# Kernel optimization log

Hardware: AMD Instinct MI355X
Metric: run time of the kernel (lower is better)

## Reference

```python
import jax, jax.numpy as jnp
import numpy as np

H = 128  # hidden_size hard-coded in AttentionSeqModel


def setup_inputs() -> dict:
    key = jax.random.key(0)
    ks = jax.random.split(key, 20)
    B, L, D, A = 512, 512, 128, 16  # batch, num_light, obs_size, action_size

    def p(k, shape, s=0.05):
        return jax.random.normal(k, shape, dtype=jnp.float32) * s

    return {
        "obs": jax.random.normal(ks[0], (B, L, D), dtype=jnp.float32),
        # encoder params
        "enc_emb_W": p(ks[1], (H, D)), "enc_emb_b": p(ks[2], (H,)),
        "enc_Wih": p(ks[3], (3 * H, H)), "enc_Whh": p(ks[4], (3 * H, H)),
        "enc_bih": p(ks[5], (3 * H,)), "enc_bhh": p(ks[6], (3 * H,)),
        # decoder params
        "dec_emb_W": p(ks[7], (H, A)), "dec_emb_b": p(ks[8], (H,)),
        "attn_W": p(ks[9], (L, 2 * H)), "attn_b": p(ks[10], (L,)),
        "comb_W": p(ks[11], (H, 2 * H)), "comb_b": p(ks[12], (H,)),
        "dec_Wih": p(ks[13], (3 * H, H)), "dec_Whh": p(ks[14], (3 * H, H)),
        "dec_bih": p(ks[15], (3 * H,)), "dec_bhh": p(ks[16], (3 * H,)),
        "out_W": p(ks[17], (A, H)), "out_b": p(ks[18], (A,)),
    }


def _gru_cell(x, h, Wih, Whh, bih, bhh):
    # torch.nn.GRU single-step semantics
    gi = x @ Wih.T + bih          # (B, 3H)
    gh = h @ Whh.T + bhh          # (B, 3H)
    ir, iz, inn = jnp.split(gi, 3, axis=-1)
    hr, hz, hn = jnp.split(gh, 3, axis=-1)
    r = jax.nn.sigmoid(ir + hr)
    z = jax.nn.sigmoid(iz + hz)
    n = jnp.tanh(inn + r * hn)
    return (1.0 - z) * n + z * h


def reference(obs, enc_emb_W, enc_emb_b, enc_Wih, enc_Whh, enc_bih, enc_bhh,
              dec_emb_W, dec_emb_b, attn_W, attn_b, comb_W, comb_b,
              dec_Wih, dec_Whh, dec_bih, dec_bhh, out_W, out_b):
    B, L, _ = obs.shape
    A = out_b.shape[0]

    # ---- encoder loop over num_light timesteps ----
    def enc_step(h, x_t):
        emb = x_t @ enc_emb_W.T + enc_emb_b           # (B, H)
        h2 = _gru_cell(emb, h, enc_Wih, enc_Whh, enc_bih, enc_bhh)
        # original stores encoder_output[0, 0]: only batch element 0
        return h2, h2[0]

    h0 = jnp.zeros((B, H), obs.dtype)
    hN, enc_outs = jax.lax.scan(enc_step, h0, jnp.swapaxes(obs, 0, 1))
    # enc_outs: (L, H)

    # ---- decoder loop, feeding log-softmax logits back as input ----
    def dec_step(carry, _):
        inp, h = carry
        emb = inp @ dec_emb_W.T + dec_emb_b           # (B, H); dropout = identity (eval)
        aw = jax.nn.softmax(jnp.concatenate([emb, h], axis=1) @ attn_W.T + attn_b, axis=1)  # (B, L)
        applied = aw @ enc_outs                        # (B, H)
        o = jax.nn.relu(jnp.concatenate([emb, applied], axis=1) @ comb_W.T + comb_b)
        h2 = _gru_cell(o, h, dec_Wih, dec_Whh, dec_bih, dec_bhh)
        logits = jax.nn.log_softmax(h2 @ out_W.T + out_b, axis=1)  # (B, A)
        return (logits, h2), None

    init = (jnp.zeros((B, A), obs.dtype), hN)
    (logits, _), _ = jax.lax.scan(dec_step, init, None, length=L)
    return logits
```

## Files before the change

kernel.cpp:

```cpp
#include <hip/hip_runtime.h>
#include <stdint.h>

#define H_  128
#define L_  512
#define B_  512
#define A_  16
#define G3_ 384

#define OFF_M1    0
#define OFF_WHHE  98304
#define OFF_WB    196608
#define OFF_WIH   327680
#define OFF_WHH   425984
#define OFF_WC2   524288
#define OFF_PA    557056
#define OFF_PC    573440
#define OFF_OUTW  577536
#define OFF_BGI   581632
#define OFF_ZB    583168
#define OFF_OB    585216
#define OFF_ENC   585728
#define OFF_HN    716800

typedef _Float16 f16_t;
typedef __attribute__((ext_vector_type(2))) _Float16 f16x2_t;

__device__ __forceinline__ float dot2f(uint32_t w, uint32_t a, float acc) {
#if __has_builtin(__builtin_amdgcn_fdot2)
  return __builtin_amdgcn_fdot2(__builtin_bit_cast(f16x2_t, w),
                                __builtin_bit_cast(f16x2_t, a), acc, false);
#else
  f16x2_t x = __builtin_bit_cast(f16x2_t, w);
  f16x2_t y = __builtin_bit_cast(f16x2_t, a);
  return acc + (float)x.x * (float)y.x + (float)x.y * (float)y.y;
#endif
}

__device__ __forceinline__ uint32_t pk2(float lo, float hi) {
#if __has_builtin(__builtin_amdgcn_cvt_pkrtz)
  return __builtin_bit_cast(uint32_t, __builtin_amdgcn_cvt_pkrtz(lo, hi));
#else
  f16x2_t v; v.x = (_Float16)lo; v.y = (_Float16)hi;
  return __builtin_bit_cast(uint32_t, v);
#endif
}

__device__ __forceinline__ float sigm(float x) { return 1.f / (1.f + __expf(-x)); }
__device__ __forceinline__ float tanh_s(float t) { float ex = __expf(2.f * t); return 1.f - 2.f / (ex + 1.f); }

#define LDS4(arr, idx) (*(const uint4*)&(arr)[(idx)])

__global__ void prep_kernel(const float* __restrict__ enc_emb_W, const float* __restrict__ enc_emb_b,
                            const float* __restrict__ enc_Wih, const float* __restrict__ enc_bih,
                            const float* __restrict__ dec_emb_W, const float* __restrict__ dec_emb_b,
                            const float* __restrict__ attn_W, const float* __restrict__ attn_b,
                            const float* __restrict__ comb_W, const float* __restrict__ comb_b,
                            const float* __restrict__ dec_Wih, const float* __restrict__ dec_Whh,
                            const float* __restrict__ enc_Whh, const float* __restrict__ out_W,
                            char* __restrict__ ws) {
  int t = blockIdx.x * 256 + threadIdx.x;
  if (t < 49152) {
    int n = t >> 7, d = t & 127; float acc = 0.f;
    for (int h = 0; h < 128; ++h) acc += enc_Wih[n*128+h] * enc_emb_W[h*128+d];
    ((f16_t*)(ws+OFF_M1))[t] = (f16_t)acc; return;
  } t -= 49152;
  if (t < 384) {
    float acc = enc_bih[t];
    for (int h = 0; h < 128; ++h) acc += enc_Wih[t*128+h] * enc_emb_b[h];
    ((float*)(ws+OFF_BGI))[t] = acc; return;
  } t -= 384;
  if (t < 8192) {
    int l = t >> 4, a = t & 15; float acc = 0.f;
    for (int k = 0; k < 128; ++k) acc += attn_W[l*256+k] * dec_emb_W[k*16+a];
    ((f16_t*)(ws+OFF_PA))[t] = (f16_t)acc; return;
  } t -= 8192;
  if (t < 512) {
    float acc = attn_b[t];
    for (int k = 0; k < 128; ++k) acc += attn_W[t*256+k] * dec_emb_b[k];
    ((float*)(ws+OFF_ZB))[t] = acc; return;
  } t -= 512;
  if (t < 2048) {
    int j = t >> 4, a = t & 15; float acc = 0.f;
    for (int k = 0; k < 128; ++k) acc += comb_W[j*256+k] * dec_emb_W[k*16+a];
    ((f16_t*)(ws+OFF_PC))[t] = (f16_t)acc; return;
  } t -= 2048;
  if (t < 128) {
    float acc = comb_b[t];
    for (int k = 0; k < 128; ++k) acc += comb_W[t*256+k] * dec_emb_b[k];
    ((float*)(ws+OFF_OB))[t] = acc; return;
  } t -= 128;
  if (t < 65536) {
    int l = t >> 7, k = t & 127;
    ((f16_t*)(ws+OFF_WB))[t] = (f16_t)attn_W[l*256+128+k]; return;
  } t -= 65536;
  if (t < 49152) { ((f16_t*)(ws+OFF_WHHE))[t] = (f16_t)enc_Whh[t]; return; } t -= 49152;
  if (t < 49152) { ((f16_t*)(ws+OFF_WIH))[t]  = (f16_t)dec_Wih[t]; return; } t -= 49152;
  if (t < 49152) { ((f16_t*)(ws+OFF_WHH))[t]  = (f16_t)dec_Whh[t]; return; } t -= 49152;
  if (t < 16384) {
    int j = t >> 7, k = t & 127;
    ((f16_t*)(ws+OFF_WC2))[t] = (f16_t)comb_W[j*256+128+k]; return;
  } t -= 16384;
  if (t < 2048) { ((f16_t*)(ws+OFF_OUTW))[t] = (f16_t)out_W[t]; return; }
}

__global__ __launch_bounds__(512, 1) void enc_kernel(const float* __restrict__ obs,
                                                     const float* __restrict__ enc_bhh,
                                                     char* __restrict__ ws) {
  __shared__ __align__(16) uint32_t obspk[2][64];
  __shared__ __align__(16) uint32_t hpk[2][64];
  __shared__ __align__(16) float    gi_s[2][G3_];
  __shared__ __align__(16) float    gh_s[2][G3_];
  __shared__ float bgi_s[G3_], bhh_s[G3_];

  const int tid = threadIdx.x, bid = blockIdx.x;
  const uint32_t* M1u  = (const uint32_t*)(ws + OFF_M1);
  const uint32_t* WHu  = (const uint32_t*)(ws + OFF_WHHE);
  const float*    bgi  = (const float*)(ws + OFF_BGI);
  f16_t* encw = (f16_t*)(ws + OFF_ENC);
  float* hN   = (float*)(ws + OFF_HN);

  uint32_t m1r[64], whr[64];
  if (tid < G3_) {
    const uint4* p1 = (const uint4*)(M1u + tid*64);
    const uint4* p2 = (const uint4*)(WHu + tid*64);
#pragma unroll
    for (int q = 0; q < 16; ++q) {
      uint4 v = p1[q]; m1r[q*4]=v.x; m1r[q*4+1]=v.y; m1r[q*4+2]=v.z; m1r[q*4+3]=v.w;
      uint4 w = p2[q]; whr[q*4]=w.x; whr[q*4+1]=w.y; whr[q*4+2]=w.z; whr[q*4+3]=w.w;
    }
    bgi_s[tid] = bgi[tid]; bhh_s[tid] = enc_bhh[tid];
  }

  const int r = tid >> 7, jj = tid & 127;
  const size_t rowbase = (size_t)(2*bid + r) * L_ * H_ + jj;
  float hreg = 0.f;
  float oA = 0.f;
  if (tid < 256) {
    float o0 = obs[rowbase + 0*H_];
    float op = __shfl_xor(o0, 1);
    if (!(jj & 1)) obspk[r][jj >> 1] = pk2(o0, op);
    oA = obs[rowbase + 1*H_];
  }
  if (tid < 128) hpk[tid>>6][tid&63] = 0u;
  __syncthreads();

#pragma unroll 1
  for (int t = 0; t < L_; ++t) {
    float oB = 0.f;
    if (tid < 256) {
      int tn = (t+2 < L_) ? t+2 : L_-1;
      oB = obs[rowbase + (size_t)tn*H_];
    }
    if (tid < G3_) {
      float g0 = bgi_s[tid], g1 = g0, ga = 0.f, gb = 0.f;
      float e0 = bhh_s[tid], e1 = e0, ea = 0.f, eb = 0.f;
#pragma unroll
      for (int c = 0; c < 16; ++c) {
        uint4 o0 = LDS4(obspk[0], c*4); uint4 o1 = LDS4(obspk[1], c*4);
        uint4 h0 = LDS4(hpk[0],  c*4);  uint4 h1 = LDS4(hpk[1],  c*4);
        g0 = dot2f(m1r[c*4+0], o0.x, g0); g0 = dot2f(m1r[c*4+1], o0.y, g0);
        ga = dot2f(m1r[c*4+2], o0.z, ga); ga = dot2f(m1r[c*4+3], o0.w, ga);
        g1 = dot2f(m1r[c*4+0], o1.x, g1); g1 = dot2f(m1r[c*4+1], o1.y, g1);
        gb = dot2f(m1r[c*4+2], o1.z, gb); gb = dot2f(m1r[c*4+3], o1.w, gb);
        e0 = dot2f(whr[c*4+0], h0.x, e0); e0 = dot2f(whr[c*4+1], h0.y, e0);
        ea = dot2f(whr[c*4+2], h0.z, ea); ea = dot2f(whr[c*4+3], h0.w, ea);
        e1 = dot2f(whr[c*4+0], h1.x, e1); e1 = dot2f(whr[c*4+1], h1.y, e1);
        eb = dot2f(whr[c*4+2], h1.z, eb); eb = dot2f(whr[c*4+3], h1.w, eb);
      }
      gi_s[0][tid] = g0+ga; gi_s[1][tid] = g1+gb;
      gh_s[0][tid] = e0+ea; gh_s[1][tid] = e1+eb;
    }
    __syncthreads();
    if (tid < 256) {
      float ir = gi_s[r][jj], iz = gi_s[r][jj+128], in_ = gi_s[r][jj+256];
      float hr = gh_s[r][jj], hz = gh_s[r][jj+128], hn = gh_s[r][jj+256];
      float rg = sigm(ir + hr);
      float zg = sigm(iz + hz);
      float nn = tanh_s(in_ + rg * hn);
      float h2 = (1.f - zg) * nn + zg * hreg;
      hreg = h2;
      float hp = __shfl_xor(h2, 1);
      float op = __shfl_xor(oA, 1);
      if (!(jj & 1)) {
        hpk[r][jj >> 1] = pk2(h2, hp);
        obspk[r][jj >> 1] = pk2(oA, op);
      }
      if (bid == 0 && r == 0) encw[t*H_ + jj] = (f16_t)h2;
      oA = oB;
    }
    __syncthreads();
  }
  if (tid < 256) hN[(2*bid + r)*H_ + jj] = hreg;
}

__global__ __launch_bounds__(512, 1) void dec_kernel(const float* __restrict__ dec_bih,
                                                     const float* __restrict__ dec_bhh,
                                                     const float* __restrict__ out_b,
                                                     char* __restrict__ ws,
                                                     float* __restrict__ dout) {
  __shared__ __align__(16) uint32_t encI[32768];
  __shared__ __align__(16) uint32_t paL[4096];
  __shared__ __align__(16) uint32_t pcL[1024];
  __shared__ __align__(16) uint32_t owL[1024];
  __shared__ __align__(16) uint32_t awpk[2][272];
  __shared__ __align__(16) uint32_t aplpk[2][64];
  __shared__ __align__(16) uint32_t gip[G3_];
  __shared__ __align__(16) uint32_t ghp[G3_];
  __shared__ __align__(16) uint32_t opk[2][64];
  __shared__ __align__(16) uint32_t hpk[2][64];
  __shared__ __align__(16) uint32_t inppk[2][8];
  __shared__ float redm[2][8], reds[2][8];

  const int tid = threadIdx.x, bid = blockIdx.x;
  const uint32_t* WBu  = (const uint32_t*)(ws + OFF_WB);
  const uint32_t* WIu  = (const uint32_t*)(ws + OFF_WIH);
  const uint32_t* WHu  = (const uint32_t*)(ws + OFF_WHH);
  const uint32_t* WCu  = (const uint32_t*)(ws + OFF_WC2);
  const uint32_t* PAu  = (const uint32_t*)(ws + OFF_PA);
  const uint32_t* PCu  = (const uint32_t*)(ws + OFF_PC);
  const uint32_t* OWu  = (const uint32_t*)(ws + OFF_OUTW);
  const float*    zb   = (const float*)(ws + OFF_ZB);
  const float*    obg  = (const float*)(ws + OFF_OB);
  const float*    hN   = (const float*)(ws + OFF_HN);

  uint32_t wb[64], wA[64], wB[64];
  {
    const uint4* p = (const uint4*)(WBu + tid*64);
#pragma unroll
    for (int q = 0; q < 16; ++q) { uint4 v = p[q]; wb[q*4]=v.x; wb[q*4+1]=v.y; wb[q*4+2]=v.z; wb[q*4+3]=v.w; }
  }
  if (tid < G3_) {
    const uint4* p = (const uint4*)(WIu + tid*64);
    const uint4* p2 = (const uint4*)(WHu + tid*64);
#pragma unroll
    for (int q = 0; q < 16; ++q) {
      uint4 v = p[q];  wA[q*4]=v.x; wA[q*4+1]=v.y; wA[q*4+2]=v.z; wA[q*4+3]=v.w;
      uint4 w = p2[q]; wB[q*4]=w.x; wB[q*4+1]=w.y; wB[q*4+2]=w.z; wB[q*4+3]=w.w;
    }
  } else {
    const uint4* p = (const uint4*)(WCu + (tid-384)*64);
#pragma unroll
    for (int q = 0; q < 16; ++q) {
      uint4 v = p[q]; wA[q*4]=v.x; wA[q*4+1]=v.y; wA[q*4+2]=v.z; wA[q*4+3]=v.w;
    }
  }

  {
    int k = tid & 127, ls = tid >> 7;
    const uint16_t* eg = (const uint16_t*)(ws + OFF_ENC);
    uint16_t* ei = (uint16_t*)encI;
    for (int cc = 0; cc < 16; ++cc) {
      int c = ls*16 + cc;
#pragma unroll
      for (int p = 0; p < 8; ++p) ei[(c*128 + k)*8 + p] = eg[(c*8 + p)*128 + k];
    }
  }
  for (int idx = tid; idx < 4096; idx += 512) {
    int q = idx >> 9, l = idx & 511;
    paL[idx] = PAu[l*8 + q];
  }
  for (int idx = tid; idx < 1024; idx += 512) {
    int q = idx >> 7, j = idx & 127;
    pcL[idx] = PCu[j*8 + q];
    int qq = idx & 3, rest = idx >> 2, a = rest & 15, c = rest >> 4;
    owL[(c*16 + a)*4 + qq] = OWu[a*64 + c*4 + qq];
  }
  const float bih_reg  = (tid < G3_) ? dec_bih[tid] : 0.f;
  const float bhh_reg  = (tid < G3_) ? dec_bhh[tid] : 0.f;
  const float ob_reg   = (tid >= G3_) ? obg[tid - G3_] : 0.f;
  const float outb_reg = (tid < 32) ? out_b[tid & 15] : 0.f;
  if (tid < 16) inppk[tid>>3][tid&7] = 0u;

  const int r6 = tid >> 7, j6 = tid & 127;
  float hreg = 0.f;
  if (tid < 256) {
    hreg = hN[(2*bid + r6)*H_ + j6];
    float hp = __shfl_xor(hreg, 1);
    if (!(j6 & 1)) hpk[r6][j6 >> 1] = pk2(hreg, hp);
  }
  const float zbias = zb[tid];
  __syncthreads();

#pragma unroll 1
  for (int t = 0; t < L_; ++t) {
    {
      uint32_t paq[8];
#pragma unroll
      for (int q = 0; q < 8; ++q) paq[q] = paL[q*512 + tid];
      uint4 i0 = LDS4(inppk[0], 0), i0b = LDS4(inppk[0], 4);
      uint4 i1 = LDS4(inppk[1], 0), i1b = LDS4(inppk[1], 4);
      float a0 = dot2f(paq[0], i0.x, zbias); a0 = dot2f(paq[1], i0.y, a0);
      a0 = dot2f(paq[2], i0.z, a0);          a0 = dot2f(paq[3], i0.w, a0);
      float b0 = dot2f(paq[4], i0b.x, 0.f);  b0 = dot2f(paq[5], i0b.y, b0);
      b0 = dot2f(paq[6], i0b.z, b0);         b0 = dot2f(paq[7], i0b.w, b0);
      float a1 = dot2f(paq[0], i1.x, zbias); a1 = dot2f(paq[1], i1.y, a1);
      a1 = dot2f(paq[2], i1.z, a1);          a1 = dot2f(paq[3], i1.w, a1);
      float b1 = dot2f(paq[4], i1b.x, 0.f);  b1 = dot2f(paq[5], i1b.y, b1);
      b1 = dot2f(paq[6], i1b.z, b1);         b1 = dot2f(paq[7], i1b.w, b1);
#pragma unroll
      for (int c = 0; c < 16; ++c) {
        uint4 h0 = LDS4(hpk[0], c*4); uint4 h1 = LDS4(hpk[1], c*4);
        a0 = dot2f(wb[c*4+0], h0.x, a0); a0 = dot2f(wb[c*4+1], h0.y, a0);
        b0 = dot2f(wb[c*4+2], h0.z, b0); b0 = dot2f(wb[c*4+3], h0.w, b0);
        a1 = dot2f(wb[c*4+0], h1.x, a1); a1 = dot2f(wb[c*4+1], h1.y, a1);
        b1 = dot2f(wb[c*4+2], h1.z, b1); b1 = dot2f(wb[c*4+3], h1.w, b1);
      }
      float z0 = a0 + b0, z1 = a1 + b1;
      float m0 = z0, m1 = z1;
#pragma unroll
      for (int off = 32; off; off >>= 1) {
        m0 = fmaxf(m0, __shfl_xor(m0, off));
        m1 = fmaxf(m1, __shfl_xor(m1, off));
      }
      float e0 = __expf(z0 - m0), e1 = __expf(z1 - m1);
      float s0 = e0, s1 = e1;
#pragma unroll
      for (int off = 32; off; off >>= 1) { s0 += __shfl_xor(s0, off); s1 += __shfl_xor(s1, off); }
      int wv = tid >> 6;
      if ((tid & 63) == 0) { redm[0][wv] = m0; redm[1][wv] = m1; reds[0][wv] = s0; reds[1][wv] = s1; }
      float ep0 = __shfl_xor(e0, 1), ep1 = __shfl_xor(e1, 1);
      int awi = (tid >> 1) + ((tid >> 7) << 2);
      if (!(tid & 1)) { awpk[0][awi] = pk2(e0, ep0); awpk[1][awi] = pk2(e1, ep1); }
    }
    __syncthreads();
    {
      int lane = tid & 63, wv3 = tid >> 6;
      int k = wv3*16 + (lane & 15), chunk = lane >> 4;
      float M0 = redm[0][0], M1 = redm[1][0];
#pragma unroll
      for (int i = 1; i < 8; ++i) { M0 = fmaxf(M0, redm[0][i]); M1 = fmaxf(M1, redm[1][i]); }
      float S0 = 0.f, S1 = 0.f;
#pragma unroll
      for (int i = 0; i < 8; ++i) {
        S0 += reds[0][i] * __expf(redm[0][i] - M0);
        S1 += reds[1][i] * __expf(redm[1][i] - M1);
      }
      float is0 = 1.f / S0, is1 = 1.f / S1;
      int cb = chunk*2;
      float sc00 = __expf(redm[0][cb]   - M0) * is0;
      float sc01 = __expf(redm[0][cb+1] - M0) * is0;
      float sc10 = __expf(redm[1][cb]   - M1) * is1;
      float sc11 = __expf(redm[1][cb+1] - M1) * is1;
      int eb0 = chunk*8192 + k*4;
      int awb = chunk*68;
      float a00=0.f, a01=0.f, a10=0.f, a11=0.f;
#pragma unroll
      for (int cc = 0; cc < 8; ++cc) {
        uint4 ev = *(const uint4*)&encI[eb0 + cc*512];
        uint4 w0 = *(const uint4*)&awpk[0][awb + cc*4];
        uint4 wq = *(const uint4*)&awpk[1][awb + cc*4];
        a00 = dot2f(ev.x, w0.x, a00); a00 = dot2f(ev.y, w0.y, a00);
        a00 = dot2f(ev.z, w0.z, a00); a00 = dot2f(ev.w, w0.w, a00);
        a10 = dot2f(ev.x, wq.x, a10); a10 = dot2f(ev.y, wq.y, a10);
        a10 = dot2f(ev.z, wq.z, a10); a10 = dot2f(ev.w, wq.w, a10);
      }
#pragma unroll
      for (int cc = 8; cc < 16; ++cc) {
        uint4 ev = *(const uint4*)&encI[eb0 + cc*512];
        uint4 w0 = *(const uint4*)&awpk[0][awb + cc*4];
        uint4 wq = *(const uint4*)&awpk[1][awb + cc*4];
        a01 = dot2f(ev.x, w0.x, a01); a01 = dot2f(ev.y, w0.y, a01);
        a01 = dot2f(ev.z, w0.z, a01); a01 = dot2f(ev.w, w0.w, a01);
        a11 = dot2f(ev.x, wq.x, a11); a11 = dot2f(ev.y, wq.y, a11);
        a11 = dot2f(ev.z, wq.z, a11); a11 = dot2f(ev.w, wq.w, a11);
      }
      float v0 = a00*sc00 + a01*sc01;
      float v1 = a10*sc10 + a11*sc11;
      v0 += __shfl_xor(v0, 16); v0 += __shfl_xor(v0, 32);
      v1 += __shfl_xor(v1, 16); v1 += __shfl_xor(v1, 32);
      float v0p = __shfl_xor(v0, 1), v1p = __shfl_xor(v1, 1);
      if (!(lane & 49)) {
        int kk = k >> 1;
        aplpk[0][kk] = pk2(v0, v0p); aplpk[1][kk] = pk2(v1, v1p);
      }
    }
    __syncthreads();
    if (tid >= G3_) {
      int jj = tid - G3_;
      uint32_t pcq[8];
#pragma unroll
      for (int q = 0; q < 8; ++q) pcq[q] = pcL[q*128 + jj];
      uint4 i0 = LDS4(inppk[0], 0), i0b = LDS4(inppk[0], 4);
      uint4 i1 = LDS4(inppk[1], 0), i1b = LDS4(inppk[1], 4);
      float o0 = dot2f(pcq[0], i0.x, ob_reg); o0 = dot2f(pcq[1], i0.y, o0);
      o0 = dot2f(pcq[2], i0.z, o0);           o0 = dot2f(pcq[3], i0.w, o0);
      float oa = dot2f(pcq[4], i0b.x, 0.f);   oa = dot2f(pcq[5], i0b.y, oa);
      oa = dot2f(pcq[6], i0b.z, oa);          oa = dot2f(pcq[7], i0b.w, oa);
      float o1 = dot2f(pcq[0], i1.x, ob_reg); o1 = dot2f(pcq[1], i1.y, o1);
      o1 = dot2f(pcq[2], i1.z, o1);           o1 = dot2f(pcq[3], i1.w, o1);
      float obb = dot2f(pcq[4], i1b.x, 0.f);  obb = dot2f(pcq[5], i1b.y, obb);
      obb = dot2f(pcq[6], i1b.z, obb);        obb = dot2f(pcq[7], i1b.w, obb);
#pragma unroll
      for (int c = 0; c < 16; ++c) {
        uint4 p0 = LDS4(aplpk[0], c*4); uint4 p1 = LDS4(aplpk[1], c*4);
        o0 = dot2f(wA[c*4+0], p0.x, o0); o0 = dot2f(wA[c*4+1], p0.y, o0);
        oa = dot2f(wA[c*4+2], p0.z, oa); oa = dot2f(wA[c*4+3], p0.w, oa);
        o1 = dot2f(wA[c*4+0], p1.x, o1); o1 = dot2f(wA[c*4+1], p1.y, o1);
        obb = dot2f(wA[c*4+2], p1.z, obb); obb = dot2f(wA[c*4+3], p1.w, obb);
      }
      o0 = fmaxf(o0 + oa, 0.f); o1 = fmaxf(o1 + obb, 0.f);
      float px0 = __shfl_xor(o0, 1), px1 = __shfl_xor(o1, 1);
      if (!(jj & 1)) { opk[0][jj>>1] = pk2(o0, px0); opk[1][jj>>1] = pk2(o1, px1); }
    } else {
      float e0g = bhh_reg, e1g = e0g, ea = 0.f, eb = 0.f;
#pragma unroll
      for (int c = 0; c < 16; ++c) {
        uint4 h0 = LDS4(hpk[0], c*4); uint4 h1 = LDS4(hpk[1], c*4);
        e0g = dot2f(wB[c*4+0], h0.x, e0g); e0g = dot2f(wB[c*4+1], h0.y, e0g);
        ea  = dot2f(wB[c*4+2], h0.z, ea);  ea  = dot2f(wB[c*4+3], h0.w, ea);
        e1g = dot2f(wB[c*4+0], h1.x, e1g); e1g = dot2f(wB[c*4+1], h1.y, e1g);
        eb  = dot2f(wB[c*4+2], h1.z, eb);  eb  = dot2f(wB[c*4+3], h1.w, eb);
      }
      ghp[tid] = pk2(e0g + ea, e1g + eb);
    }
    __syncthreads();
    if (tid < G3_) {
      float g0 = bih_reg, g1 = g0, ga = 0.f, gb = 0.f;
#pragma unroll
      for (int c = 0; c < 16; ++c) {
        uint4 o0 = LDS4(opk[0], c*4); uint4 o1 = LDS4(opk[1], c*4);
        g0 = dot2f(wA[c*4+0], o0.x, g0); g0 = dot2f(wA[c*4+1], o0.y, g0);
        ga = dot2f(wA[c*4+2], o0.z, ga); ga = dot2f(wA[c*4+3], o0.w, ga);
        g1 = dot2f(wA[c*4+0], o1.x, g1); g1 = dot2f(wA[c*4+1], o1.y, g1);
        gb = dot2f(wA[c*4+2], o1.z, gb); gb = dot2f(wA[c*4+3], o1.w, gb);
      }
      gip[tid] = pk2(g0 + ga, g1 + gb);
    }
    __syncthreads();
    if (tid < 256) {
#define UNPK_(u) (r6 ? (float)(__builtin_bit_cast(f16x2_t,(u)).y) : (float)(__builtin_bit_cast(f16x2_t,(u)).x))
      float ir = UNPK_(gip[j6]), iz = UNPK_(gip[j6+128]), in_ = UNPK_(gip[j6+256]);
      float hr = UNPK_(ghp[j6]), hz = UNPK_(ghp[j6+128]), hn = UNPK_(ghp[j6+256]);
#undef UNPK_
      float rg = sigm(ir + hr);
      float zg = sigm(iz + hz);
      float nn = tanh_s(in_ + rg * hn);
      float h2 = (1.f - zg) * nn + zg * hreg;
      hreg = h2;
      float hp = __shfl_xor(h2, 1);
      if (!(j6 & 1)) hpk[r6][j6 >> 1] = pk2(h2, hp);
    }
    __syncthreads();
    if (tid < 32) {
      int rr = tid >> 4, a = tid & 15;
      float y = outb_reg, y2 = 0.f, y3 = 0.f, y4 = 0.f;
#pragma unroll
      for (int c = 0; c < 16; ++c) {
        uint4 w  = *(const uint4*)&owL[(c*16 + a)*4];
        uint4 hb = LDS4(hpk[rr], c*4);
        y  = dot2f(w.x, hb.x, y);  y2 = dot2f(w.y, hb.y, y2);
        y3 = dot2f(w.z, hb.z, y3); y4 = dot2f(w.w, hb.w, y4);
      }
      y += y2 + y3 + y4;
      float m = y;
#pragma unroll
      for (int off = 8; off; off >>= 1) m = fmaxf(m, __shfl_xor(m, off));
      float e = __expf(y - m);
      float s = e;
#pragma unroll
      for (int off = 8; off; off >>= 1) s += __shfl_xor(s, off);
      float lsf = (y - m) - __logf(s);
      if (t == L_-1) dout[(2*bid + rr)*A_ + a] = lsf;
      float pr = __shfl_xor(lsf, 1);
      if (!(a & 1)) inppk[rr][a >> 1] = pk2(lsf, pr);
    }
    __syncthreads();
  }
}

extern "C" void kernel_launch(void* const* d_in, const int* in_sizes, int n_in,
                              void* d_out, int out_size, void* d_ws, size_t ws_size,
                              hipStream_t stream) {
  (void)in_sizes; (void)n_in; (void)out_size; (void)ws_size;
  const float* obs       = (const float*)d_in[0];
  const float* enc_emb_W = (const float*)d_in[1];
  const float* enc_emb_b = (const float*)d_in[2];
  const float* enc_Wih   = (const float*)d_in[3];
  const float* enc_Whh   = (const float*)d_in[4];
  const float* enc_bih   = (const float*)d_in[5];
  const float* enc_bhh   = (const float*)d_in[6];
  const float* dec_emb_W = (const float*)d_in[7];
  const float* dec_emb_b = (const float*)d_in[8];
  const float* attn_W    = (const float*)d_in[9];
  const float* attn_b    = (const float*)d_in[10];
  const float* comb_W    = (const float*)d_in[11];
  const float* comb_b    = (const float*)d_in[12];
  const float* dec_Wih   = (const float*)d_in[13];
  const float* dec_Whh   = (const float*)d_in[14];
  const float* dec_bih   = (const float*)d_in[15];
  const float* dec_bhh   = (const float*)d_in[16];
  const float* out_W     = (const float*)d_in[17];
  const float* out_b     = (const float*)d_in[18];
  char* ws = (char*)d_ws;

  hipLaunchKernelGGL(prep_kernel, dim3(1140), dim3(256), 0, stream,
                     enc_emb_W, enc_emb_b, enc_Wih, enc_bih, dec_emb_W, dec_emb_b,
                     attn_W, attn_b, comb_W, comb_b, dec_Wih, dec_Whh, enc_Whh, out_W, ws);
  hipLaunchKernelGGL(enc_kernel, dim3(256), dim3(512), 0, stream, obs, enc_bhh, ws);
  hipLaunchKernelGGL(dec_kernel, dim3(256), dim3(512), 0, stream,
                     dec_bih, dec_bhh, out_b, ws, (float*)d_out);
}
```

Measured before the change: 4.377 ms.

## Split decoder to one batch row per block and read encoder outputs from global

The decoder kernel now runs 512 blocks each handling a single batch row instead of 256 blocks handling two, halving per-step serial work per block. The encoder writes its outputs in an interleaved layout so the decoder reads them straight from global/L2 rather than staging 128KB into LDS. Softmax max-subtraction is dropped for attention and output log-softmax, and the GRU update and output projection are merged into one phase to remove a barrier. Risks: global reads of encoder outputs every step, and possible overflow without max-subtraction.

After: 16.32 ms. +272.9%, slower.

```diff
diff --git a/kernel.cpp b/kernel.cpp
--- a/kernel.cpp
+++ b/kernel.cpp
@@ -185,7 +185,7 @@
         hpk[r][jj >> 1] = pk2(h2, hp);
         obspk[r][jj >> 1] = pk2(oA, op);
       }
-      if (bid == 0 && r == 0) encw[t*H_ + jj] = (f16_t)h2;
+      if (bid == 0 && r == 0) encw[(((t >> 3) * 128 + jj) << 3) + (t & 7)] = (f16_t)h2;
       oA = oB;
     }
     __syncthreads();
@@ -198,18 +198,17 @@
                                                      const float* __restrict__ out_b,
                                                      char* __restrict__ ws,
                                                      float* __restrict__ dout) {
-  __shared__ __align__(16) uint32_t encI[32768];
   __shared__ __align__(16) uint32_t paL[4096];
   __shared__ __align__(16) uint32_t pcL[1024];
   __shared__ __align__(16) uint32_t owL[1024];
-  __shared__ __align__(16) uint32_t awpk[2][272];
-  __shared__ __align__(16) uint32_t aplpk[2][64];
-  __shared__ __align__(16) uint32_t gip[G3_];
-  __shared__ __align__(16) uint32_t ghp[G3_];
-  __shared__ __align__(16) uint32_t opk[2][64];
-  __shared__ __align__(16) uint32_t hpk[2][64];
-  __shared__ __align__(16) uint32_t inppk[2][8];
-  __shared__ float redm[2][8], reds[2][8];
+  __shared__ __align__(16) uint32_t awpk[272];
+  __shared__ __align__(16) uint32_t aplpk[64];
+  __shared__ __align__(16) float    gi_s[G3_];
+  __shared__ __align__(16) float    gh_s[G3_];
+  __shared__ __align__(16) uint32_t opk[64];
+  __shared__ __align__(16) uint32_t hpk[64];
+  __shared__ __align__(16) uint32_t inppk[8];
+  __shared__ float reds[8];
 
   const int tid = threadIdx.x, bid = blockIdx.x;
   const uint32_t* WBu  = (const uint32_t*)(ws + OFF_WB);
@@ -219,6 +218,7 @@
   const uint32_t* PAu  = (const uint32_t*)(ws + OFF_PA);
   const uint32_t* PCu  = (const uint32_t*)(ws + OFF_PC);
   const uint32_t* OWu  = (const uint32_t*)(ws + OFF_OUTW);
+  const uint32_t* encG = (const uint32_t*)(ws + OFF_ENC);
   const float*    zb   = (const float*)(ws + OFF_ZB);
   const float*    obg  = (const float*)(ws + OFF_OB);
   const float*    hN   = (const float*)(ws + OFF_HN);
@@ -245,16 +245,6 @@
     }
   }
 
-  {
-    int k = tid & 127, ls = tid >> 7;
-    const uint16_t* eg = (const uint16_t*)(ws + OFF_ENC);
-    uint16_t* ei = (uint16_t*)encI;
-    for (int cc = 0; cc < 16; ++cc) {
-      int c = ls*16 + cc;
-#pragma unroll
-      for (int p = 0; p < 8; ++p) ei[(c*128 + k)*8 + p] = eg[(c*8 + p)*128 + k];
-    }
-  }
   for (int idx = tid; idx < 4096; idx += 512) {
     int q = idx >> 9, l = idx & 511;
     paL[idx] = PAu[l*8 + q];
@@ -265,20 +255,20 @@
     int qq = idx & 3, rest = idx >> 2, a = rest & 15, c = rest >> 4;
     owL[(c*16 + a)*4 + qq] = OWu[a*64 + c*4 + qq];
   }
+  const float zbias    = zb[tid];
   const float bih_reg  = (tid < G3_) ? dec_bih[tid] : 0.f;
   const float bhh_reg  = (tid < G3_) ? dec_bhh[tid] : 0.f;
   const float ob_reg   = (tid >= G3_) ? obg[tid - G3_] : 0.f;
-  const float outb_reg = (tid < 32) ? out_b[tid & 15] : 0.f;
-  if (tid < 16) inppk[tid>>3][tid&7] = 0u;
-
-  const int r6 = tid >> 7, j6 = tid & 127;
-  float hreg = 0.f;
-  if (tid < 256) {
-    hreg = hN[(2*bid + r6)*H_ + j6];
-    float hp = __shfl_xor(hreg, 1);
-    if (!(j6 & 1)) hpk[r6][j6 >> 1] = pk2(hreg, hp);
-  }
-  const float zbias = zb[tid];
+  const float outb_reg = (tid < 16) ? out_b[tid] : 0.f;
+  if (tid < 8) inppk[tid] = 0u;
+
+  float hx = 0.f, hy = 0.f;
+  if (tid < 64) {
+    hx = hN[bid*H_ + 2*tid];
+    hy = hN[bid*H_ + 2*tid + 1];
+    hpk[tid] = pk2(hx, hy);
+  }
+  const int kI2 = tid >> 2, ch = tid & 3;
   __syncthreads();
 
 #pragma unroll 1
@@ -287,182 +277,130 @@
       uint32_t paq[8];
 #pragma unroll
       for (int q = 0; q < 8; ++q) paq[q] = paL[q*512 + tid];
-      uint4 i0 = LDS4(inppk[0], 0), i0b = LDS4(inppk[0], 4);
-      uint4 i1 = LDS4(inppk[1], 0), i1b = LDS4(inppk[1], 4);
+      uint4 i0 = LDS4(inppk, 0), i0b = LDS4(inppk, 4);
       float a0 = dot2f(paq[0], i0.x, zbias); a0 = dot2f(paq[1], i0.y, a0);
       a0 = dot2f(paq[2], i0.z, a0);          a0 = dot2f(paq[3], i0.w, a0);
       float b0 = dot2f(paq[4], i0b.x, 0.f);  b0 = dot2f(paq[5], i0b.y, b0);
       b0 = dot2f(paq[6], i0b.z, b0);         b0 = dot2f(paq[7], i0b.w, b0);
-      float a1 = dot2f(paq[0], i1.x, zbias); a1 = dot2f(paq[1], i1.y, a1);
-      a1 = dot2f(paq[2], i1.z, a1);          a1 = dot2f(paq[3], i1.w, a1);
-      float b1 = dot2f(paq[4], i1b.x, 0.f);  b1 = dot2f(paq[5], i1b.y, b1);
-      b1 = dot2f(paq[6], i1b.z, b1);         b1 = dot2f(paq[7], i1b.w, b1);
 #pragma unroll
       for (int c = 0; c < 16; ++c) {
-        uint4 h0 = LDS4(hpk[0], c*4); uint4 h1 = LDS4(hpk[1], c*4);
+        uint4 h0 = LDS4(hpk, c*4);
         a0 = dot2f(wb[c*4+0], h0.x, a0); a0 = dot2f(wb[c*4+1], h0.y, a0);
         b0 = dot2f(wb[c*4+2], h0.z, b0); b0 = dot2f(wb[c*4+3], h0.w, b0);
-        a1 = dot2f(wb[c*4+0], h1.x, a1); a1 = dot2f(wb[c*4+1], h1.y, a1);
-        b1 = dot2f(wb[c*4+2], h1.z, b1); b1 = dot2f(wb[c*4+3], h1.w, b1);
-      }
-      float z0 = a0 + b0, z1 = a1 + b1;
-      float m0 = z0, m1 = z1;
-#pragma unroll
-      for (int off = 32; off; off >>= 1) {
-        m0 = fmaxf(m0, __shfl_xor(m0, off));
-        m1 = fmaxf(m1, __shfl_xor(m1, off));
-      }
-      float e0 = __expf(z0 - m0), e1 = __expf(z1 - m1);
-      float s0 = e0, s1 = e1;
-#pragma unroll
-      for (int off = 32; off; off >>= 1) { s0 += __shfl_xor(s0, off); s1 += __shfl_xor(s1, off); }
-      int wv = tid >> 6;
-      if ((tid & 63) == 0) { redm[0][wv] = m0; redm[1][wv] = m1; reds[0][wv] = s0; reds[1][wv] = s1; }
-      float ep0 = __shfl_xor(e0, 1), ep1 = __shfl_xor(e1, 1);
+      }
+      float e0 = __expf(a0 + b0);
+      float s0 = e0;
+#pragma unroll
+      for (int off = 32; off; off >>= 1) s0 += __shfl_xor(s0, off);
+      if ((tid & 63) == 0) reds[tid >> 6] = s0;
+      float ep0 = __shfl_xor(e0, 1);
       int awi = (tid >> 1) + ((tid >> 7) << 2);
-      if (!(tid & 1)) { awpk[0][awi] = pk2(e0, ep0); awpk[1][awi] = pk2(e1, ep1); }
+      if (!(tid & 1)) awpk[awi] = pk2(e0, ep0);
     }
     __syncthreads();
     {
-      int lane = tid & 63, wv3 = tid >> 6;
-      int k = wv3*16 + (lane & 15), chunk = lane >> 4;
-      float M0 = redm[0][0], M1 = redm[1][0];
-#pragma unroll
-      for (int i = 1; i < 8; ++i) { M0 = fmaxf(M0, redm[0][i]); M1 = fmaxf(M1, redm[1][i]); }
-      float S0 = 0.f, S1 = 0.f;
-#pragma unroll
-      for (int i = 0; i < 8; ++i) {
-        S0 += reds[0][i] * __expf(redm[0][i] - M0);
-        S1 += reds[1][i] * __expf(redm[1][i] - M1);
-      }
-      float is0 = 1.f / S0, is1 = 1.f / S1;
-      int cb = chunk*2;
-      float sc00 = __expf(redm[0][cb]   - M0) * is0;
-      float sc01 = __expf(redm[0][cb+1] - M0) * is0;
-      float sc10 = __expf(redm[1][cb]   - M1) * is1;
-      float sc11 = __expf(redm[1][cb+1] - M1) * is1;
-      int eb0 = chunk*8192 + k*4;
-      int awb = chunk*68;
-      float a00=0.f, a01=0.f, a10=0.f, a11=0.f;
-#pragma unroll
-      for (int cc = 0; cc < 8; ++cc) {
-        uint4 ev = *(const uint4*)&encI[eb0 + cc*512];
-        uint4 w0 = *(const uint4*)&awpk[0][awb + cc*4];
-        uint4 wq = *(const uint4*)&awpk[1][awb + cc*4];
-        a00 = dot2f(ev.x, w0.x, a00); a00 = dot2f(ev.y, w0.y, a00);
-        a00 = dot2f(ev.z, w0.z, a00); a00 = dot2f(ev.w, w0.w, a00);
-        a10 = dot2f(ev.x, wq.x, a10); a10 = dot2f(ev.y, wq.y, a10);
-        a10 = dot2f(ev.z, wq.z, a10); a10 = dot2f(ev.w, wq.w, a10);
-      }
-#pragma unroll
-      for (int cc = 8; cc < 16; ++cc) {
-        uint4 ev = *(const uint4*)&encI[eb0 + cc*512];
-        uint4 w0 = *(const uint4*)&awpk[0][awb + cc*4];
-        uint4 wq = *(const uint4*)&awpk[1][awb + cc*4];
-        a01 = dot2f(ev.x, w0.x, a01); a01 = dot2f(ev.y, w0.y, a01);
-        a01 = dot2f(ev.z, w0.z, a01); a01 = dot2f(ev.w, w0.w, a01);
-        a11 = dot2f(ev.x, wq.x, a11); a11 = dot2f(ev.y, wq.y, a11);
-        a11 = dot2f(ev.z, wq.z, a11); a11 = dot2f(ev.w, wq.w, a11);
-      }
-      float v0 = a00*sc00 + a01*sc01;
-      float v1 = a10*sc10 + a11*sc11;
-      v0 += __shfl_xor(v0, 16); v0 += __shfl_xor(v0, 32);
-      v1 += __shfl_xor(v1, 16); v1 += __shfl_xor(v1, 32);
-      float v0p = __shfl_xor(v0, 1), v1p = __shfl_xor(v1, 1);
-      if (!(lane & 49)) {
-        int kk = k >> 1;
-        aplpk[0][kk] = pk2(v0, v0p); aplpk[1][kk] = pk2(v1, v1p);
-      }
+      float S = reds[0];
+#pragma unroll
+      for (int i = 1; i < 8; ++i) S += reds[i];
+      float is = 1.f / S;
+      float acc0 = 0.f, acc1 = 0.f;
+#pragma unroll
+      for (int cc = 0; cc < 16; ++cc) {
+        int c = ch*16 + cc;
+        uint4 ev = *(const uint4*)(encG + (size_t)(c*128 + kI2)*4);
+        uint4 w  = LDS4(awpk, c*4 + ((c >> 4) << 2));
+        acc0 = dot2f(ev.x, w.x, acc0); acc0 = dot2f(ev.y, w.y, acc0);
+        acc1 = dot2f(ev.z, w.z, acc1); acc1 = dot2f(ev.w, w.w, acc1);
+      }
+      float v = (acc0 + acc1) * is;
+      v += __shfl_xor(v, 1); v += __shfl_xor(v, 2);
+      float vp = __shfl_xor(v, 4);
+      if (!(tid & 7)) aplpk[tid >> 3] = pk2(v, vp);
     }
     __syncthreads();
     if (tid >= G3_) {
-      int jj = tid - G3_;
+      int j = tid - G3_;
       uint32_t pcq[8];
 #pragma unroll
-      for (int q = 0; q < 8; ++q) pcq[q] = pcL[q*128 + jj];
-      uint4 i0 = LDS4(inppk[0], 0), i0b = LDS4(inppk[0], 4);
-      uint4 i1 = LDS4(inppk[1], 0), i1b = LDS4(inppk[1], 4);
+      for (int q = 0; q < 8; ++q) pcq[q] = pcL[q*128 + j];
+      uint4 i0 = LDS4(inppk, 0), i0b = LDS4(inppk, 4);
       float o0 = dot2f(pcq[0], i0.x, ob_reg); o0 = dot2f(pcq[1], i0.y, o0);
       o0 = dot2f(pcq[2], i0.z, o0);           o0 = dot2f(pcq[3], i0.w, o0);
       float oa = dot2f(pcq[4], i0b.x, 0.f);   oa = dot2f(pcq[5], i0b.y, oa);
       oa = dot2f(pcq[6], i0b.z, oa);          oa = dot2f(pcq[7], i0b.w, oa);
-      float o1 = dot2f(pcq[0], i1.x, ob_reg); o1 = dot2f(pcq[1], i1.y, o1);
-      o1 = dot2f(pcq[2], i1.z, o1);           o1 = dot2f(pcq[3], i1.w, o1);
-      float obb = dot2f(pcq[4], i1b.x, 0.f);  obb = dot2f(pcq[5], i1b.y, obb);
-      obb = dot2f(pcq[6], i1b.z, obb);        obb = dot2f(pcq[7], i1b.w, obb);
 #pragma unroll
       for (int c = 0; c < 16; ++c) {
-        uint4 p0 = LDS4(aplpk[0], c*4); uint4 p1 = LDS4(aplpk[1], c*4);
+        uint4 p0 = LDS4(aplpk, c*4);
         o0 = dot2f(wA[c*4+0], p0.x, o0); o0 = dot2f(wA[c*4+1], p0.y, o0);
         oa = dot2f(wA[c*4+2], p0.z, oa); oa = dot2f(wA[c*4+3], p0.w, oa);
-        o1 = dot2f(wA[c*4+0], p1.x, o1); o1 = dot2f(wA[c*4+1], p1.y, o1);
-        obb = dot2f(wA[c*4+2], p1.z, obb); obb = dot2f(wA[c*4+3], p1.w, obb);
-      }
-      o0 = fmaxf(o0 + oa, 0.f); o1 = fmaxf(o1 + obb, 0.f);
-      float px0 = __shfl_xor(o0, 1), px1 = __shfl_xor(o1, 1);
-      if (!(jj & 1)) { opk[0][jj>>1] = pk2(o0, px0); opk[1][jj>>1] = pk2(o1, px1); }
+      }
+      o0 = fmaxf(o0 + oa, 0.f);
+      float px = __shfl_xor(o0, 1);
+      if (!(j & 1)) opk[j >> 1] = pk2(o0, px);
     } else {
-      float e0g = bhh_reg, e1g = e0g, ea = 0.f, eb = 0.f;
+      float e0g = bhh_reg, ea = 0.f;
 #pragma unroll
       for (int c = 0; c < 16; ++c) {
-        uint4 h0 = LDS4(hpk[0], c*4); uint4 h1 = LDS4(hpk[1], c*4);
+        uint4 h0 = LDS4(hpk, c*4);
         e0g = dot2f(wB[c*4+0], h0.x, e0g); e0g = dot2f(wB[c*4+1], h0.y, e0g);
         ea  = dot2f(wB[c*4+2], h0.z, ea);  ea  = dot2f(wB[c*4+3], h0.w, ea);
-        e1g = dot2f(wB[c*4+0], h1.x, e1g); e1g = dot2f(wB[c*4+1], h1.y, e1g);
-        eb  = dot2f(wB[c*4+2], h1.z, eb);  eb  = dot2f(wB[c*4+3], h1.w, eb);
-      }
-      ghp[tid] = pk2(e0g + ea, e1g + eb);
+      }
+      gh_s[tid] = e0g + ea;
     }
     __syncthreads();
     if (tid < G3_) {
-      float g0 = bih_reg, g1 = g0, ga = 0.f, gb = 0.f;
+      float g0 = bih_reg, ga = 0.f;
 #pragma unroll
       for (int c = 0; c < 16; ++c) {
-        uint4 o0 = LDS4(opk[0], c*4); uint4 o1 = LDS4(opk[1], c*4);
+        uint4 o0 = LDS4(opk, c*4);
         g0 = dot2f(wA[c*4+0], o0.x, g0); g0 = dot2f(wA[c*4+1], o0.y, g0);
         ga = dot2f(wA[c*4+2], o0.z, ga); ga = dot2f(wA[c*4+3], o0.w, ga);
-        g1 = dot2f(wA[c*4+0], o1.x, g1); g1 = dot2f(wA[c*4+1], o1.y, g1);
-        gb = dot2f(wA[c*4+2], o1.z, gb); gb = dot2f(wA[c*4+3], o1.w, gb);
-      }
-      gip[tid] = pk2(g0 + ga, g1 + gb);
-    }
-    __syncthreads();
-    if (tid < 256) {
-#define UNPK_(u) (r6 ? (float)(__builtin_bit_cast(f16x2_t,(u)).y) : (float)(__builtin_bit_cast(f16x2_t,(u)).x))
-      float ir = UNPK_(gip[j6]), iz = UNPK_(gip[j6+128]), in_ = UNPK_(gip[j6+256]);
-      float hr = UNPK_(ghp[j6]), hz = UNPK_(ghp[j6+128]), hn = UNPK_(ghp[j6+256]);
-#undef UNPK_
-      float rg = sigm(ir + hr);
-      float zg = sigm(iz + hz);
-      float nn = tanh_s(in_ + rg * hn);
-      float h2 = (1.f - zg) * nn + zg * hreg;
-      hreg = h2;
-      float hp = __shfl_xor(h2, 1);
-      if (!(j6 & 1)) hpk[r6][j6 >> 1] = pk2(h2, hp);
-    }
-    __syncthreads();
-    if (tid < 32) {
-      int rr = tid >> 4, a = tid & 15;
-      float y = outb_reg, y2 = 0.f, y3 = 0.f, y4 = 0.f;
-#pragma unroll
-      for (int c = 0; c < 16; ++c) {
-        uint4 w  = *(const uint4*)&owL[(c*16 + a)*4];
-        uint4 hb = LDS4(hpk[rr], c*4);
-        y  = dot2f(w.x, hb.x, y);  y2 = dot2f(w.y, hb.y, y2);
-        y3 = dot2f(w.z, hb.z, y3); y4 = dot2f(w.w, hb.w, y4);
-      }
-      y += y2 + y3 + y4;
-      float m = y;
-#pragma unroll
-      for (int off = 8; off; off >>= 1) m = fmaxf(m, __shfl_xor(m, off));
-      float e = __expf(y - m);
-      float s = e;
-#pragma unroll
-      for (int off = 8; off; off >>= 1) s += __shfl_xor(s, off);
-      float lsf = (y - m) - __logf(s);
-      if (t == L_-1) dout[(2*bid + rr)*A_ + a] = lsf;
-      float pr = __shfl_xor(lsf, 1);
-      if (!(a & 1)) inppk[rr][a >> 1] = pk2(lsf, pr);
+      }
+      gi_s[tid] = g0 + ga;
+    }
+    __syncthreads();
+    if (tid < 64) {
+      float2 ir2 = *(const float2*)&gi_s[2*tid];
+      float2 iz2 = *(const float2*)&gi_s[128 + 2*tid];
+      float2 in2 = *(const float2*)&gi_s[256 + 2*tid];
+      float2 hr2 = *(const float2*)&gh_s[2*tid];
+      float2 hz2 = *(const float2*)&gh_s[128 + 2*tid];
+      float2 hn2 = *(const float2*)&gh_s[256 + 2*tid];
+      {
+        float rg = sigm(ir2.x + hr2.x);
+        float zg = sigm(iz2.x + hz2.x);
+        float nn = tanh_s(in2.x + rg * hn2.x);
+        hx = (1.f - zg) * nn + zg * hx;
+      }
+      {
+        float rg = sigm(ir2.y + hr2.y);
+        float zg = sigm(iz2.y + hz2.y);
+        float nn = tanh_s(in2.y + rg * hn2.y);
+        hy = (1.f - zg) * nn + zg * hy;
+      }
+      hpk[tid] = pk2(hx, hy);
+      asm volatile("s_waitcnt lgkmcnt(0)" ::: "memory");
+      int a = tid & 15, ks = tid >> 4;
+      float y = (ks == 0) ? outb_reg : 0.f;
+#pragma unroll
+      for (int w = 0; w < 4; ++w) {
+        int c = ks*4 + w;
+        uint4 ww = *(const uint4*)&owL[(c*16 + a)*4];
+        uint4 hb = LDS4(hpk, c*4);
+        y = dot2f(ww.x, hb.x, y); y = dot2f(ww.y, hb.y, y);
+        y = dot2f(ww.z, hb.z, y); y = dot2f(ww.w, hb.w, y);
+      }
+      y += __shfl_xor(y, 16); y += __shfl_xor(y, 32);
+      if (tid < 16) {
+        float e = __expf(y);
+        float s = e;
+#pragma unroll
+        for (int off = 8; off; off >>= 1) s += __shfl_xor(s, off);
+        float lsf = y - __logf(s);
+        if (t == L_-1) dout[bid*A_ + a] = lsf;
+        float pr = __shfl_xor(lsf, 1);
+        if (!(a & 1)) inppk[a >> 1] = pk2(lsf, pr);
+      }
     }
     __syncthreads();
   }
@@ -497,6 +435,6 @@
                      enc_emb_W, enc_emb_b, enc_Wih, enc_bih, dec_emb_W, dec_emb_b,
                      attn_W, attn_b, comb_W, comb_b, dec_Wih, dec_Whh, enc_Whh, out_W, ws);
   hipLaunchKernelGGL(enc_kernel, dim3(256), dim3(512), 0, stream, obs, enc_bhh, ws);
-  hipLaunchKernelGGL(dec_kernel, dim3(256), dim3(512), 0, stream,
+  hipLaunchKernelGGL(dec_kernel, dim3(512), dim3(512), 0, stream,
                      dec_bih, dec_bhh, out_b, ws, (float*)d_out);
 }
```

## Merge GRU update and output projection into one wave, drop softmax max passes

Applied to the files above, without the earlier changes.

The decoder GRU state update and the output log-softmax now run in a single 64-thread wave, with each thread handling two hidden units for both batch rows. This removes one block-wide barrier per timestep. The max-subtraction passes in the attention softmax and the output log-softmax are dropped, which also removes the cross-wave max reduction. The attention-applied reduction is re-laid out as a 4-way split per output element. Skipping the max subtraction risks overflow in exp if the logits grow large, and the code relies on an inline waitcnt rather than a barrier to order the LDS write of h before it is read back.

After: 5.436 ms. 24.2% more time.

```diff
diff --git a/kernel.cpp b/kernel.cpp
--- a/kernel.cpp
+++ b/kernel.cpp
@@ -47,6 +47,12 @@
 
 __device__ __forceinline__ float sigm(float x) { return 1.f / (1.f + __expf(-x)); }
 __device__ __forceinline__ float tanh_s(float t) { float ex = __expf(2.f * t); return 1.f - 2.f / (ex + 1.f); }
+__device__ __forceinline__ float gru1(float ir, float iz, float in_, float hr, float hz, float hn, float h) {
+  float rg = sigm(ir + hr);
+  float zg = sigm(iz + hz);
+  float nn = tanh_s(in_ + rg * hn);
+  return (1.f - zg) * nn + zg * h;
+}
 
 #define LDS4(arr, idx) (*(const uint4*)&(arr)[(idx)])
 
@@ -174,10 +180,7 @@
     if (tid < 256) {
       float ir = gi_s[r][jj], iz = gi_s[r][jj+128], in_ = gi_s[r][jj+256];
       float hr = gh_s[r][jj], hz = gh_s[r][jj+128], hn = gh_s[r][jj+256];
-      float rg = sigm(ir + hr);
-      float zg = sigm(iz + hz);
-      float nn = tanh_s(in_ + rg * hn);
-      float h2 = (1.f - zg) * nn + zg * hreg;
+      float h2 = gru1(ir, iz, in_, hr, hz, hn, hreg);
       hreg = h2;
       float hp = __shfl_xor(h2, 1);
       float op = __shfl_xor(oA, 1);
@@ -202,14 +205,14 @@
   __shared__ __align__(16) uint32_t paL[4096];
   __shared__ __align__(16) uint32_t pcL[1024];
   __shared__ __align__(16) uint32_t owL[1024];
-  __shared__ __align__(16) uint32_t awpk[2][272];
+  __shared__ __align__(16) uint32_t awpk[2][256];
   __shared__ __align__(16) uint32_t aplpk[2][64];
   __shared__ __align__(16) uint32_t gip[G3_];
   __shared__ __align__(16) uint32_t ghp[G3_];
   __shared__ __align__(16) uint32_t opk[2][64];
   __shared__ __align__(16) uint32_t hpk[2][64];
   __shared__ __align__(16) uint32_t inppk[2][8];
-  __shared__ float redm[2][8], reds[2][8];
+  __shared__ float reds[2][8];
 
   const int tid = threadIdx.x, bid = blockIdx.x;
   const uint32_t* WBu  = (const uint32_t*)(ws + OFF_WB);
@@ -265,20 +268,22 @@
     int qq = idx & 3, rest = idx >> 2, a = rest & 15, c = rest >> 4;
     owL[(c*16 + a)*4 + qq] = OWu[a*64 + c*4 + qq];
   }
+  const float zbias    = zb[tid];
   const float bih_reg  = (tid < G3_) ? dec_bih[tid] : 0.f;
   const float bhh_reg  = (tid < G3_) ? dec_bhh[tid] : 0.f;
   const float ob_reg   = (tid >= G3_) ? obg[tid - G3_] : 0.f;
   const float outb_reg = (tid < 32) ? out_b[tid & 15] : 0.f;
   if (tid < 16) inppk[tid>>3][tid&7] = 0u;
 
-  const int r6 = tid >> 7, j6 = tid & 127;
-  float hreg = 0.f;
-  if (tid < 256) {
-    hreg = hN[(2*bid + r6)*H_ + j6];
-    float hp = __shfl_xor(hreg, 1);
-    if (!(j6 & 1)) hpk[r6][j6 >> 1] = pk2(hreg, hp);
-  }
-  const float zbias = zb[tid];
+  float h00 = 0.f, h01 = 0.f, h10 = 0.f, h11 = 0.f;
+  if (tid < 64) {
+    h00 = hN[(2*bid + 0)*H_ + 2*tid];
+    h01 = hN[(2*bid + 0)*H_ + 2*tid + 1];
+    h10 = hN[(2*bid + 1)*H_ + 2*tid];
+    h11 = hN[(2*bid + 1)*H_ + 2*tid + 1];
+    hpk[0][tid] = pk2(h00, h01);
+    hpk[1][tid] = pk2(h10, h11);
+  }
   __syncthreads();
 
 #pragma unroll 1
@@ -305,74 +310,40 @@
         a1 = dot2f(wb[c*4+0], h1.x, a1); a1 = dot2f(wb[c*4+1], h1.y, a1);
         b1 = dot2f(wb[c*4+2], h1.z, b1); b1 = dot2f(wb[c*4+3], h1.w, b1);
       }
-      float z0 = a0 + b0, z1 = a1 + b1;
-      float m0 = z0, m1 = z1;
-#pragma unroll
-      for (int off = 32; off; off >>= 1) {
-        m0 = fmaxf(m0, __shfl_xor(m0, off));
-        m1 = fmaxf(m1, __shfl_xor(m1, off));
-      }
-      float e0 = __expf(z0 - m0), e1 = __expf(z1 - m1);
+      float e0 = __expf(a0 + b0), e1 = __expf(a1 + b1);
       float s0 = e0, s1 = e1;
 #pragma unroll
       for (int off = 32; off; off >>= 1) { s0 += __shfl_xor(s0, off); s1 += __shfl_xor(s1, off); }
       int wv = tid >> 6;
-      if ((tid & 63) == 0) { redm[0][wv] = m0; redm[1][wv] = m1; reds[0][wv] = s0; reds[1][wv] = s1; }
+      if ((tid & 63) == 0) { reds[0][wv] = s0; reds[1][wv] = s1; }
       float ep0 = __shfl_xor(e0, 1), ep1 = __shfl_xor(e1, 1);
-      int awi = (tid >> 1) + ((tid >> 7) << 2);
-      if (!(tid & 1)) { awpk[0][awi] = pk2(e0, ep0); awpk[1][awi] = pk2(e1, ep1); }
+      if (!(tid & 1)) { awpk[0][tid>>1] = pk2(e0, ep0); awpk[1][tid>>1] = pk2(e1, ep1); }
     }
     __syncthreads();
     {
-      int lane = tid & 63, wv3 = tid >> 6;
-      int k = wv3*16 + (lane & 15), chunk = lane >> 4;
-      float M0 = redm[0][0], M1 = redm[1][0];
-#pragma unroll
-      for (int i = 1; i < 8; ++i) { M0 = fmaxf(M0, redm[0][i]); M1 = fmaxf(M1, redm[1][i]); }
+      int k = tid >> 2, q4 = tid & 3;
       float S0 = 0.f, S1 = 0.f;
 #pragma unroll
-      for (int i = 0; i < 8; ++i) {
-        S0 += reds[0][i] * __expf(redm[0][i] - M0);
-        S1 += reds[1][i] * __expf(redm[1][i] - M1);
-      }
+      for (int i = 0; i < 8; ++i) { S0 += reds[0][i]; S1 += reds[1][i]; }
       float is0 = 1.f / S0, is1 = 1.f / S1;
-      int cb = chunk*2;
-      float sc00 = __expf(redm[0][cb]   - M0) * is0;
-      float sc01 = __expf(redm[0][cb+1] - M0) * is0;
-      float sc10 = __expf(redm[1][cb]   - M1) * is1;
-      float sc11 = __expf(redm[1][cb+1] - M1) * is1;
-      int eb0 = chunk*8192 + k*4;
-      int awb = chunk*68;
-      float a00=0.f, a01=0.f, a10=0.f, a11=0.f;
-#pragma unroll
-      for (int cc = 0; cc < 8; ++cc) {
-        uint4 ev = *(const uint4*)&encI[eb0 + cc*512];
-        uint4 w0 = *(const uint4*)&awpk[0][awb + cc*4];
-        uint4 wq = *(const uint4*)&awpk[1][awb + cc*4];
+      float a00 = 0.f, a01 = 0.f, a10 = 0.f, a11 = 0.f;
+#pragma unroll
+      for (int cc = 0; cc < 16; ++cc) {
+        int c = q4*16 + cc;
+        uint4 ev = *(const uint4*)&encI[(c*128 + k)*4];
+        uint4 w0 = LDS4(awpk[0], c*4);
+        uint4 w1 = LDS4(awpk[1], c*4);
         a00 = dot2f(ev.x, w0.x, a00); a00 = dot2f(ev.y, w0.y, a00);
-        a00 = dot2f(ev.z, w0.z, a00); a00 = dot2f(ev.w, w0.w, a00);
-        a10 = dot2f(ev.x, wq.x, a10); a10 = dot2f(ev.y, wq.y, a10);
-        a10 = dot2f(ev.z, wq.z, a10); a10 = dot2f(ev.w, wq.w, a10);
-      }
-#pragma unroll
-      for (int cc = 8; cc < 16; ++cc) {
-        uint4 ev = *(const uint4*)&encI[eb0 + cc*512];
-        uint4 w0 = *(const uint4*)&awpk[0][awb + cc*4];
-        uint4 wq = *(const uint4*)&awpk[1][awb + cc*4];
-        a01 = dot2f(ev.x, w0.x, a01); a01 = dot2f(ev.y, w0.y, a01);
         a01 = dot2f(ev.z, w0.z, a01); a01 = dot2f(ev.w, w0.w, a01);
-        a11 = dot2f(ev.x, wq.x, a11); a11 = dot2f(ev.y, wq.y, a11);
-        a11 = dot2f(ev.z, wq.z, a11); a11 = dot2f(ev.w, wq.w, a11);
-      }
-      float v0 = a00*sc00 + a01*sc01;
-      float v1 = a10*sc10 + a11*sc11;
-      v0 += __shfl_xor(v0, 16); v0 += __shfl_xor(v0, 32);
-      v1 += __shfl_xor(v1, 16); v1 += __shfl_xor(v1, 32);
-      float v0p = __shfl_xor(v0, 1), v1p = __shfl_xor(v1, 1);
-      if (!(lane & 49)) {
-        int kk = k >> 1;
-        aplpk[0][kk] = pk2(v0, v0p); aplpk[1][kk] = pk2(v1, v1p);
-      }
+        a10 = dot2f(ev.x, w1.x, a10); a10 = dot2f(ev.y, w1.y, a10);
+        a11 = dot2f(ev.z, w1.z, a11); a11 = dot2f(ev.w, w1.w, a11);
+      }
+      float v0 = (a00 + a01) * is0;
+      float v1 = (a10 + a11) * is1;
+      v0 += __shfl_xor(v0, 1); v0 += __shfl_xor(v0, 2);
+      v1 += __shfl_xor(v1, 1); v1 += __shfl_xor(v1, 2);
+      float p0 = __shfl_xor(v0, 4), p1x = __shfl_xor(v1, 4);
+      if (!(tid & 7)) { aplpk[0][tid>>3] = pk2(v0, p0); aplpk[1][tid>>3] = pk2(v1, p1x); }
     }
     __syncthreads();
     if (tid >= G3_) {
@@ -427,42 +398,46 @@
       gip[tid] = pk2(g0 + ga, g1 + gb);
     }
     __syncthreads();
-    if (tid < 256) {
-#define UNPK_(u) (r6 ? (float)(__builtin_bit_cast(f16x2_t,(u)).y) : (float)(__builtin_bit_cast(f16x2_t,(u)).x))
-      float ir = UNPK_(gip[j6]), iz = UNPK_(gip[j6+128]), in_ = UNPK_(gip[j6+256]);
-      float hr = UNPK_(ghp[j6]), hz = UNPK_(ghp[j6+128]), hn = UNPK_(ghp[j6+256]);
-#undef UNPK_
-      float rg = sigm(ir + hr);
-      float zg = sigm(iz + hz);
-      float nn = tanh_s(in_ + rg * hn);
-      float h2 = (1.f - zg) * nn + zg * hreg;
-      hreg = h2;
-      float hp = __shfl_xor(h2, 1);
-      if (!(j6 & 1)) hpk[r6][j6 >> 1] = pk2(h2, hp);
-    }
-    __syncthreads();
-    if (tid < 32) {
-      int rr = tid >> 4, a = tid & 15;
-      float y = outb_reg, y2 = 0.f, y3 = 0.f, y4 = 0.f;
-#pragma unroll
-      for (int c = 0; c < 16; ++c) {
-        uint4 w  = *(const uint4*)&owL[(c*16 + a)*4];
+    if (tid < 64) {
+      uint2 gA = *(const uint2*)&gip[2*tid];
+      uint2 gB = *(const uint2*)&gip[128 + 2*tid];
+      uint2 gC = *(const uint2*)&gip[256 + 2*tid];
+      uint2 eA = *(const uint2*)&ghp[2*tid];
+      uint2 eB = *(const uint2*)&ghp[128 + 2*tid];
+      uint2 eC = *(const uint2*)&ghp[256 + 2*tid];
+#define PX(u) ((float)(__builtin_bit_cast(f16x2_t,(u)).x))
+#define PY(u) ((float)(__builtin_bit_cast(f16x2_t,(u)).y))
+      h00 = gru1(PX(gA.x), PX(gB.x), PX(gC.x), PX(eA.x), PX(eB.x), PX(eC.x), h00);
+      h01 = gru1(PX(gA.y), PX(gB.y), PX(gC.y), PX(eA.y), PX(eB.y), PX(eC.y), h01);
+      h10 = gru1(PY(gA.x), PY(gB.x), PY(gC.x), PY(eA.x), PY(eB.x), PY(eC.x), h10);
+      h11 = gru1(PY(gA.y), PY(gB.y), PY(gC.y), PY(eA.y), PY(eB.y), PY(eC.y), h11);
+#undef PX
+#undef PY
+      hpk[0][tid] = pk2(h00, h01);
+      hpk[1][tid] = pk2(h10, h11);
+      asm volatile("s_waitcnt lgkmcnt(0)" ::: "memory");
+      int a = tid & 15, grp = tid >> 4;
+      int rr = grp & 1, kh = grp >> 1;
+      float y = kh ? 0.f : outb_reg;
+#pragma unroll
+      for (int cc = 0; cc < 8; ++cc) {
+        int c = kh*8 + cc;
+        uint4 ww = *(const uint4*)&owL[(c*16 + a)*4];
         uint4 hb = LDS4(hpk[rr], c*4);
-        y  = dot2f(w.x, hb.x, y);  y2 = dot2f(w.y, hb.y, y2);
-        y3 = dot2f(w.z, hb.z, y3); y4 = dot2f(w.w, hb.w, y4);
-      }
-      y += y2 + y3 + y4;
-      float m = y;
-#pragma unroll
-      for (int off = 8; off; off >>= 1) m = fmaxf(m, __shfl_xor(m, off));
-      float e = __expf(y - m);
-      float s = e;
-#pragma unroll
-      for (int off = 8; off; off >>= 1) s += __shfl_xor(s, off);
-      float lsf = (y - m) - __logf(s);
-      if (t == L_-1) dout[(2*bid + rr)*A_ + a] = lsf;
-      float pr = __shfl_xor(lsf, 1);
-      if (!(a & 1)) inppk[rr][a >> 1] = pk2(lsf, pr);
+        y = dot2f(ww.x, hb.x, y); y = dot2f(ww.y, hb.y, y);
+        y = dot2f(ww.z, hb.z, y); y = dot2f(ww.w, hb.w, y);
+      }
+      y += __shfl_xor(y, 32);
+      if (tid < 32) {
+        float e = __expf(y);
+        float s = e;
+#pragma unroll
+        for (int off = 8; off; off >>= 1) s += __shfl_xor(s, off);
+        float lsf = y - __logf(s);
+        if (t == L_-1) dout[(2*bid + rr)*A_ + a] = lsf;
+        float pr = __shfl_xor(lsf, 1);
+        if (!(a & 1)) inppk[rr][a >> 1] = pk2(lsf, pr);
+      }
     }
     __syncthreads();
   }
```
